# Optimization experiments

Measured on AMD Instinct MI355X. Metric: run time of the kernel, lower is better.

Reference implementation:

```python
import jax, jax.numpy as jnp
import numpy as np

N = 100000          # total nodes
E = 1200000         # total edges
IN_CH = 22          # NUM_NODES_SINGLE_TEAM * 2
HID = 64
NUM_CLASSES = 3
G = 256             # graphs in batch


def setup_inputs() -> dict:
    key = jax.random.key(0)
    ks = jax.random.split(key, 12)
    x = jax.random.normal(ks[0], (N, IN_CH), jnp.float32)
    edge_index = jax.random.randint(ks[1], (2, E), 0, N, dtype=jnp.int32)
    edge_weight = jax.random.uniform(ks[2], (E,), jnp.float32)
    batch = jnp.sort(jax.random.randint(ks[3], (N,), 0, G, dtype=jnp.int32))

    def lin_w(k, fi, fo):
        return jax.random.normal(k, (fi, fo), jnp.float32) / np.float32(np.sqrt(fi))

    return {
        "x": x,
        "edge_index": edge_index,
        "edge_weight": edge_weight,
        "batch": batch,
        "W1": lin_w(ks[4], IN_CH, HID),  "b1": jnp.zeros((HID,), jnp.float32),
        "W2": lin_w(ks[5], HID, HID),    "b2": jnp.zeros((HID,), jnp.float32),
        "fw1": lin_w(ks[6], HID, HID),   "fb1": jnp.zeros((HID,), jnp.float32),
        "fw2": lin_w(ks[7], HID, NUM_CLASSES), "fb2": jnp.zeros((NUM_CLASSES,), jnp.float32),
    }


def gcn_conv(x, edge_index, edge_weight, W, b):
    """PyG GCNConv: self-loops (weight 1) + symmetric normalization + scatter-add."""
    n = x.shape[0]
    loop = jnp.arange(n, dtype=edge_index.dtype)
    row = jnp.concatenate([edge_index[0], loop])
    col = jnp.concatenate([edge_index[1], loop])
    w = jnp.concatenate([edge_weight, jnp.ones((n,), x.dtype)])
    deg = jax.ops.segment_sum(w, col, num_segments=n)        # weighted in-degree
    safe = jnp.where(deg > 0, deg, 1.0)
    dinv = jnp.where(deg > 0, jax.lax.rsqrt(safe), 0.0)
    norm = dinv[row] * w * dinv[col]                         # [E+N]
    h = x @ W                                                # transform first (d small)
    msg = norm[:, None] * h[row]                             # gather + scale
    out = jax.ops.segment_sum(msg, col, num_segments=n)      # scatter-add
    return out + b


def reference(x, edge_index, edge_weight, batch, W1, b1, W2, b2, fw1, fb1, fw2, fb2):
    h = jax.nn.relu(gcn_conv(x, edge_index, edge_weight, W1, b1))
    h = jax.nn.relu(gcn_conv(h, edge_index, edge_weight, W2, b2))
    # global_mean_pool
    sums = jax.ops.segment_sum(h, batch, num_segments=G)
    cnt = jax.ops.segment_sum(jnp.ones((h.shape[0],), h.dtype), batch, num_segments=G)
    pooled = sums / jnp.maximum(cnt, 1.0)[:, None]
    h = jax.nn.relu(pooled @ fw1 + fb1)
    return h @ fw2 + fb2
```

## Files before the change

### kernel.cpp

```cpp
#include <hip/hip_runtime.h>
#include <hip/hip_bf16.h>
#include <hip/hip_fp16.h>


#define HIDC 64
#define MTILE 128
#define XS_STRIDE (MTILE + 4)
#define BSHIFT 9
#define SPAN 512
#define NBKT_MAX 256
#define BCHUNK 2048

typedef unsigned long long u64;

__global__ void k_init(int* bucket_cnt, int nb, float* pooled, int npool) {
    int i = blockIdx.x * blockDim.x + threadIdx.x;
    if (i < nb) bucket_cnt[i] = 0;
    if (i < npool) pooled[i] = 0.f;
}

__global__ __launch_bounds__(256) void k_bin_count(const int* __restrict__ col,
                                                   int* bucket_cnt, int E, int NB) {
    __shared__ int hist[NBKT_MAX];
    int tid = threadIdx.x;
    for (int i = tid; i < NB; i += 256) hist[i] = 0;
    __syncthreads();
    int base = blockIdx.x * 8192;
    for (int j = 0; j < 32; ++j) {
        int e = base + j * 256 + tid;
        if (e < E) atomicAdd(&hist[col[e] >> BSHIFT], 1);
    }
    __syncthreads();
    for (int i = tid; i < NB; i += 256)
        if (hist[i]) atomicAdd(&bucket_cnt[i], hist[i]);
}

__global__ void k_bucket_scan(const int* __restrict__ bucket_cnt, int* __restrict__ bucket_base,
                              int* __restrict__ cursor_g, int NB, int E) {
    __shared__ int s[256];
    int t = threadIdx.x;
    int v = (t < NB) ? bucket_cnt[t] : 0;
    s[t] = v;
    __syncthreads();
    for (int o = 1; o < 256; o <<= 1) {
        int x = (t >= o) ? s[t - o] : 0;
        __syncthreads();
        s[t] += x;
        __syncthreads();
    }
    if (t < NB) { int ex = s[t] - v; bucket_base[t] = ex; cursor_g[t] = ex; }
    if (t == 0) bucket_base[NB] = E;
}

__global__ __launch_bounds__(256) void k_bin_scatter(const int* __restrict__ row,
                                                     const int* __restrict__ col,
                                                     const float* __restrict__ ew,
                                                     int* cursor_g, u64* __restrict__ bedges,
                                                     int E, int NB) {
    __shared__ int hist[NBKT_MAX], binoff[NBKT_MAX], cursor[NBKT_MAX], gbase[NBKT_MAX];
    __shared__ int s[256];
    __shared__ u64 stage[BCHUNK];
    __shared__ unsigned char binid[BCHUNK];
    int tid = threadIdx.x;
    for (int i = tid; i < NB; i += 256) hist[i] = 0;
    __syncthreads();
    int base = blockIdx.x * BCHUNK;
    u64 pk[8]; int bb[8];
#pragma unroll
    for (int j = 0; j < 8; ++j) {
        int e = base + j * 256 + tid;
        if (e < E) {
            int c = col[e];
            bb[j] = c >> BSHIFT;
            pk[j] = ((u64)__float_as_uint(ew[e]) << 32) |
                    ((u64)(unsigned)row[e] << BSHIFT) | (unsigned)(c & (SPAN - 1));
            atomicAdd(&hist[bb[j]], 1);
        } else bb[j] = -1;
    }
    __syncthreads();
    {
        int v = (tid < NB) ? hist[tid] : 0;
        s[tid] = v;
        __syncthreads();
        for (int o = 1; o < 256; o <<= 1) {
            int x = (tid >= o) ? s[tid - o] : 0;
            __syncthreads();
            s[tid] += x;
            __syncthreads();
        }
        if (tid < NB) { binoff[tid] = s[tid] - v; cursor[tid] = s[tid] - v; }
    }
    __syncthreads();
#pragma unroll
    for (int j = 0; j < 8; ++j)
        if (bb[j] >= 0) {
            int pos = atomicAdd(&cursor[bb[j]], 1);
            stage[pos] = pk[j];
            binid[pos] = (unsigned char)bb[j];
        }
    __syncthreads();
    if (tid < NB && hist[tid] > 0) gbase[tid] = atomicAdd(&cursor_g[tid], hist[tid]);
    __syncthreads();
    int total = min(BCHUNK, E - base);
    for (int i = tid; i < total; i += 256) {
        int b = binid[i];
        bedges[(size_t)gbase[b] + (i - binoff[b])] = stage[i];
    }
}

__global__ __launch_bounds__(256) void k_bucket_process(const u64* __restrict__ bedges,
                                                        const int* __restrict__ bucket_base,
                                                        const float* __restrict__ x,
                                                        u64* __restrict__ csr,
                                                        float* __restrict__ dinv,
                                                        int* __restrict__ off,
                                                        __half* __restrict__ x16,
                                                        int N, int E, int NB, int K) {
    __shared__ float deg[SPAN];
    __shared__ int cL[SPAN];
    __shared__ int offL[SPAN];
    __shared__ int s[256];
    int b = blockIdx.x, tid = threadIdx.x;
    int ebase = bucket_base[b], ecnt = bucket_base[b + 1] - ebase;
    int nd0 = b << BSHIFT;
    int ndn = min(SPAN, N - nd0);
    for (int i = tid; i < SPAN; i += 256) { deg[i] = 1.0f; cL[i] = 0; }
    __syncthreads();
    for (int e = tid; e < ecnt; e += 256) {
        u64 p = bedges[ebase + e];
        int colin = (int)(p & (SPAN - 1));
        atomicAdd(&deg[colin], __uint_as_float((unsigned)(p >> 32)));
        atomicAdd(&cL[colin], 1);
    }
    __syncthreads();
    int p0 = cL[2 * tid], p1 = cL[2 * tid + 1];
    s[tid] = p0 + p1;
    __syncthreads();
    for (int o = 1; o < 256; o <<= 1) {
        int x_ = (tid >= o) ? s[tid - o] : 0;
        __syncthreads();
        s[tid] += x_;
        __syncthreads();
    }
    int ex = s[tid] - (p0 + p1);
    offL[2 * tid] = ex;
    offL[2 * tid + 1] = ex + p0;
    __syncthreads();
    for (int i = tid; i < ndn; i += 256) {
        float dv = rsqrtf(deg[i]);
        deg[i] = dv;
        dinv[nd0 + i] = dv;
        off[nd0 + i] = ebase + offL[i];
    }
    for (int i = tid; i < SPAN; i += 256) cL[i] = offL[i];
    if (b == NB - 1 && tid == 0) off[N] = E;
    __syncthreads();
    for (int e = tid; e < ecnt; e += 256) {
        u64 p = bedges[ebase + e];
        int colin = (int)(p & (SPAN - 1));
        int src = (int)((p >> BSHIFT) & 0x7FFFFF);
        int slot = atomicAdd(&cL[colin], 1);
        csr[(size_t)ebase + slot] = ((u64)(unsigned)src << 32) | (unsigned)(p >> 32);
    }
    for (int i = tid; i < ndn * 16; i += 256) {
        int nl = i >> 4, p = i & 15, c0 = p * 2;
        float dv = deg[nl];
        const float* xr = x + (size_t)(nd0 + nl) * K;
        float a = (c0 < K)     ? dv * xr[c0]     : 0.f;
        float bq = (c0 + 1 < K) ? dv * xr[c0 + 1] : 0.f;
        reinterpret_cast<__half2*>(x16)[(size_t)(nd0 + nl) * 16 + p] = __floats2half2_rn(a, bq);
    }
}

__global__ void k_agg_x(const __half* __restrict__ x16, const int* __restrict__ off,
                        const u64* __restrict__ csr, const float* __restrict__ dinv,
                        float* __restrict__ agg, int n, int K) {
    int t = blockIdx.x * blockDim.x + threadIdx.x;
    int lane = threadIdx.x & 63;
    int node = ((t >> 6) << 3) + (lane >> 3);
    int sub = lane & 7;
    if (node >= n) return;
    const uint2* xp = reinterpret_cast<const uint2*>(x16);
    uint2 sv = xp[(size_t)node * 8 + sub];
    float acc0, acc1, acc2, acc3;
    {
        float2 a = __half22float2(*(const __half2*)&sv.x);
        float2 b = __half22float2(*(const __half2*)&sv.y);
        acc0 = a.x; acc1 = a.y; acc2 = b.x; acc3 = b.y;
    }
    int i = off[node], e1 = off[node + 1];
    for (; i + 7 < e1; i += 8) {
        u64 e[8]; uint2 r[8];
#pragma unroll
        for (int j = 0; j < 8; ++j) e[j] = csr[i + j];
#pragma unroll
        for (int j = 0; j < 8; ++j) r[j] = xp[(size_t)(e[j] >> 32) * 8 + sub];
#pragma unroll
        for (int j = 0; j < 8; ++j) {
            float w = __uint_as_float((unsigned)e[j]);
            float2 a = __half22float2(*(const __half2*)&r[j].x);
            float2 b = __half22float2(*(const __half2*)&r[j].y);
            acc0 = fmaf(w, a.x, acc0); acc1 = fmaf(w, a.y, acc1);
            acc2 = fmaf(w, b.x, acc2); acc3 = fmaf(w, b.y, acc3);
        }
    }
    for (; i < e1; ++i) {
        u64 e0 = csr[i];
        uint2 r = xp[(size_t)(e0 >> 32) * 8 + sub];
        float w = __uint_as_float((unsigned)e0);
        float2 a = __half22float2(*(const __half2*)&r.x);
        float2 b = __half22float2(*(const __half2*)&r.y);
        acc0 = fmaf(w, a.x, acc0); acc1 = fmaf(w, a.y, acc1);
        acc2 = fmaf(w, b.x, acc2); acc3 = fmaf(w, b.y, acc3);
    }
    int c0 = sub * 4;
    float d = dinv[node];
    float* ap = agg + (size_t)node * K + c0;
    if (c0 + 3 < K) {
        float2 o0; o0.x = d * acc0; o0.y = d * acc1;
        float2 o1; o1.x = d * acc2; o1.y = d * acc3;
        *reinterpret_cast<float2*>(ap) = o0;
        *reinterpret_cast<float2*>(ap + 2) = o1;
    } else if (c0 < K) {
        float2 o; o.x = d * acc0; o.y = d * acc1;
        *reinterpret_cast<float2*>(ap) = o;
    }
}

template <int K1>
__global__ __launch_bounds__(256) void k_layer1_fused(const float* __restrict__ agg,
                                                      const float* __restrict__ W1,
                                                      const float* __restrict__ b1,
                                                      const float* __restrict__ W2,
                                                      const float* __restrict__ dinv,
                                                      __half* __restrict__ h, int n) {
    __shared__ float smem[HIDC * XS_STRIDE];
    __shared__ float ws[HIDC * HIDC];
    int tid = threadIdx.x;
    int n0 = blockIdx.x * MTILE;

    for (int i = tid; i < K1 * HIDC; i += 256) ws[i] = W1[i];
    for (int i = tid; i < MTILE * K1; i += 256) {
        int r = i / K1, k = i - r * K1;
        smem[k * XS_STRIDE + r] = (n0 + r < n) ? agg[(size_t)(n0 + r) * K1 + k] : 0.f;
    }
    __syncthreads();

    int c0 = (tid & 15) * 4;
    int m0 = (tid >> 4) * 8;
    float acc[8][4];
#pragma unroll
    for (int j = 0; j < 8; ++j)
#pragma unroll
        for (int q = 0; q < 4; ++q) acc[j][q] = 0.f;

#pragma unroll 2
    for (int k = 0; k < K1; ++k) {
        float4 a0 = *reinterpret_cast<const float4*>(&smem[k * XS_STRIDE + m0]);
        float4 a1 = *reinterpret_cast<const float4*>(&smem[k * XS_STRIDE + m0 + 4]);
        float4 b  = *reinterpret_cast<const float4*>(&ws[k * HIDC + c0]);
        float av[8] = {a0.x, a0.y, a0.z, a0.w, a1.x, a1.y, a1.z, a1.w};
        float bv[4] = {b.x, b.y, b.z, b.w};
#pragma unroll
        for (int j = 0; j < 8; ++j)
#pragma unroll
            for (int q = 0; q < 4; ++q)
                acc[j][q] = fmaf(av[j], bv[q], acc[j][q]);
    }

    float4 bb = *reinterpret_cast<const float4*>(b1 + c0);
    float bv4[4] = {bb.x, bb.y, bb.z, bb.w};
#pragma unroll
    for (int j = 0; j < 8; ++j)
#pragma unroll
        for (int q = 0; q < 4; ++q)
            acc[j][q] = fmaxf(acc[j][q] + bv4[q], 0.f);

    __syncthreads();

#pragma unroll
    for (int j = 0; j < 8; ++j)
#pragma unroll
        for (int q = 0; q < 4; ++q)
            smem[(c0 + q) * XS_STRIDE + (m0 + j)] = (n0 + m0 + j < n) ? acc[j][q] : 0.f;
    for (int i = tid; i < HIDC * HIDC; i += 256) ws[i] = W2[i];
    __syncthreads();

#pragma unroll
    for (int j = 0; j < 8; ++j)
#pragma unroll
        for (int q = 0; q < 4; ++q) acc[j][q] = 0.f;

#pragma unroll 2
    for (int k = 0; k < HIDC; ++k) {
        float4 a0 = *reinterpret_cast<const float4*>(&smem[k * XS_STRIDE + m0]);
        float4 a1 = *reinterpret_cast<const float4*>(&smem[k * XS_STRIDE + m0 + 4]);
        float4 b  = *reinterpret_cast<const float4*>(&ws[k * HIDC + c0]);
        float av[8] = {a0.x, a0.y, a0.z, a0.w, a1.x, a1.y, a1.z, a1.w};
        float bv[4] = {b.x, b.y, b.z, b.w};
#pragma unroll
        for (int j = 0; j < 8; ++j)
#pragma unroll
            for (int q = 0; q < 4; ++q)
                acc[j][q] = fmaf(av[j], bv[q], acc[j][q]);
    }

#pragma unroll
    for (int j = 0; j < 8; ++j) {
        int node = n0 + m0 + j;
        if (node < n) {
            float dv = dinv[node];
            union { struct { __half2 a, b; } h2; float2 f2; } u;
            u.h2.a = __floats2half2_rn(acc[j][0] * dv, acc[j][1] * dv);
            u.h2.b = __floats2half2_rn(acc[j][2] * dv, acc[j][3] * dv);
            *reinterpret_cast<float2*>(h + (size_t)node * HIDC + c0) = u.f2;
        }
    }
}

__global__ void k_gcn_gather(const __half* __restrict__ h, const int* __restrict__ off,
                             const u64* __restrict__ csr, const float* __restrict__ dinv,
                             const float* __restrict__ bias, float* __restrict__ out, int n) {
    int t = blockIdx.x * blockDim.x + threadIdx.x;
    int lane = threadIdx.x & 63;
    int node = ((t >> 6) << 2) + (lane >> 4);
    int sub = lane & 15;
    if (node >= n) return;
    const uint2* hp = reinterpret_cast<const uint2*>(h);
    float d = dinv[node];
    uint2 sv = hp[(size_t)node * 16 + sub];
    float acc0, acc1, acc2, acc3;
    {
        float2 a = __half22float2(*(const __half2*)&sv.x);
        float2 b = __half22float2(*(const __half2*)&sv.y);
        acc0 = a.x; acc1 = a.y; acc2 = b.x; acc3 = b.y;
    }
    int i = off[node], e1 = off[node + 1];
    for (; i + 7 < e1; i += 8) {
        u64 e[8]; uint2 r[8];
#pragma unroll
        for (int j = 0; j < 8; ++j) e[j] = csr[i + j];
#pragma unroll
        for (int j = 0; j < 8; ++j) r[j] = hp[(size_t)(e[j] >> 32) * 16 + sub];
#pragma unroll
        for (int j = 0; j < 8; ++j) {
            float w = __uint_as_float((unsigned)e[j]);
            float2 a = __half22float2(*(const __half2*)&r[j].x);
            float2 b = __half22float2(*(const __half2*)&r[j].y);
            acc0 = fmaf(w, a.x, acc0); acc1 = fmaf(w, a.y, acc1);
            acc2 = fmaf(w, b.x, acc2); acc3 = fmaf(w, b.y, acc3);
        }
    }
    for (; i < e1; ++i) {
        u64 e0 = csr[i];
        uint2 r = hp[(size_t)(e0 >> 32) * 16 + sub];
        float w = __uint_as_float((unsigned)e0);
        float2 a = __half22float2(*(const __half2*)&r.x);
        float2 b = __half22float2(*(const __half2*)&r.y);
        acc0 = fmaf(w, a.x, acc0); acc1 = fmaf(w, a.y, acc1);
        acc2 = fmaf(w, b.x, acc2); acc3 = fmaf(w, b.y, acc3);
    }
    int c0 = sub * 4;
    float4 bb = *reinterpret_cast<const float4*>(bias + c0);
    float4 o;
    o.x = fmaxf(fmaf(d, acc0, bb.x), 0.f);
    o.y = fmaxf(fmaf(d, acc1, bb.y), 0.f);
    o.z = fmaxf(fmaf(d, acc2, bb.z), 0.f);
    o.w = fmaxf(fmaf(d, acc3, bb.w), 0.f);
    *reinterpret_cast<float4*>(out + (size_t)node * HIDC + c0) = o;
}

__global__ void k_pool(const float* __restrict__ h, const int* __restrict__ batch,
                       float* __restrict__ pooled, float* __restrict__ cnt, int n) {
    int c = threadIdx.x & 63, sub = threadIdx.x >> 6;
    int n0 = blockIdx.x * 256;
    int nend = min(n0 + 256, n);
    float acc = 0.f, cacc = 0.f;
    int curb = -1;
    for (int i = n0 + sub; i < nend; i += 4) {
        int b = batch[i];
        if (b != curb) {
            if (curb >= 0) {
                atomicAdd(&pooled[curb * HIDC + c], acc);
                if (c == 0) atomicAdd(&cnt[curb], cacc);
            }
            acc = 0.f; cacc = 0.f;
            curb = b;
        }
        acc += h[(size_t)i * HIDC + c];
        cacc += 1.f;
    }
    if (curb >= 0) {
        atomicAdd(&pooled[curb * HIDC + c], acc);
        if (c == 0) atomicAdd(&cnt[curb], cacc);
    }
}

__global__ void k_head(const float* __restrict__ pooled, const float* __restrict__ cnt,
                       const float* __restrict__ fw1, const float* __restrict__ fb1,
                       const float* __restrict__ fw2, const float* __restrict__ fb2,
                       float* __restrict__ out, int nclass) {
    int g = blockIdx.x;
    int j = threadIdx.x;
    __shared__ float p[HIDC], hid[HIDC];
    float c = fmaxf(cnt[g], 1.0f);
    p[j] = pooled[g * HIDC + j] / c;
    __syncthreads();
    float acc = fb1[j];
#pragma unroll 8
    for (int k = 0; k < HIDC; ++k) acc = fmaf(p[k], fw1[k * HIDC + j], acc);
    hid[j] = fmaxf(acc, 0.f);
    __syncthreads();
    if (j < nclass) {
        float o = fb2[j];
#pragma unroll 8
        for (int k = 0; k < HIDC; ++k) o = fmaf(hid[k], fw2[k * nclass + j], o);
        out[g * nclass + j] = o;
    }
}

extern "C" void kernel_launch(void* const* d_in, const int* in_sizes, int n_in,
                              void* d_out, int out_size, void* d_ws, size_t ws_size,
                              hipStream_t stream) {
    const float* x    = (const float*)d_in[0];
    const int* eidx   = (const int*)d_in[1];
    const float* ew   = (const float*)d_in[2];
    const int* batch  = (const int*)d_in[3];
    const float* W1   = (const float*)d_in[4];
    const float* b1   = (const float*)d_in[5];
    const float* W2   = (const float*)d_in[6];
    const float* b2   = (const float*)d_in[7];
    const float* fw1  = (const float*)d_in[8];
    const float* fb1  = (const float*)d_in[9];
    const float* fw2  = (const float*)d_in[10];
    const float* fb2  = (const float*)d_in[11];
    float* out = (float*)d_out;

    const int N = in_sizes[3];
    const int E = in_sizes[1] / 2;
    const int INCH = in_sizes[0] / N;
    const int NCLASS = in_sizes[11];
    const int G = out_size / NCLASS;
    const int NB = (N + SPAN - 1) >> BSHIFT;

    const int* row = eidx;
    const int* col = eidx + E;

    char* wp = (char*)d_ws;
    u64*   bedges = (u64*)wp;    wp += sizeof(u64) * E;
    u64*   csr    = (u64*)wp;    wp += sizeof(u64) * E;
    float* dinv   = (float*)wp;  wp += sizeof(float) * N;
    __half* x16   = (__half*)wp; wp += sizeof(__half) * (size_t)N * 32;
    float* agg    = (float*)wp;  wp += sizeof(float) * (size_t)N * INCH;
    __half* hbuf  = (__half*)wp; wp += sizeof(__half) * (size_t)N * HIDC;
    float* bufB   = (float*)wp;  wp += sizeof(float) * (size_t)N * HIDC;
    float* pooled = (float*)wp;  wp += sizeof(float) * (size_t)G * HIDC;
    float* cnt    = (float*)wp;  wp += sizeof(float) * G;
    int*   off    = (int*)wp;    wp += sizeof(int) * (N + 1);
    int*   bucket_cnt  = (int*)wp; wp += sizeof(int) * NBKT_MAX;
    int*   bucket_base = (int*)wp; wp += sizeof(int) * (NBKT_MAX + 1);
    int*   cursor_g    = (int*)wp; wp += sizeof(int) * NBKT_MAX;

    const int BLK = 256;
    dim3 blk(BLK);
    int gTile   = (N + MTILE - 1) / MTILE;
    int gAggX   = (N + 31) / 32;
    int gGather = (N + 15) / 16;
    int nInit   = max(NB, G * HIDC + G);

    k_init<<<(nInit + BLK - 1) / BLK, blk, 0, stream>>>(bucket_cnt, NB, pooled, G * HIDC + G);

    k_bin_count<<<(E + 8191) / 8192, blk, 0, stream>>>(col, bucket_cnt, E, NB);
    k_bucket_scan<<<1, blk, 0, stream>>>(bucket_cnt, bucket_base, cursor_g, NB, E);
    k_bin_scatter<<<(E + BCHUNK - 1) / BCHUNK, blk, 0, stream>>>(row, col, ew, cursor_g,
                                                                 bedges, E, NB);
    k_bucket_process<<<NB, blk, 0, stream>>>(bedges, bucket_base, x, csr, dinv, off, x16,
                                             N, E, NB, INCH);

    k_agg_x<<<gAggX, blk, 0, stream>>>(x16, off, csr, dinv, agg, N, INCH);
    k_layer1_fused<22><<<gTile, blk, 0, stream>>>(agg, W1, b1, W2, dinv, hbuf, N);

    k_gcn_gather<<<gGather, blk, 0, stream>>>(hbuf, off, csr, dinv, b2, bufB, N);

    k_pool<<<(N + 255) / 256, blk, 0, stream>>>(bufB, batch, pooled, cnt, N);
    k_head<<<G, dim3(64), 0, stream>>>(pooled, cnt, fw1, fb1, fw2, fb2, out, NCLASS);
}
```

Baseline: 201.6 us.

## Halve bucket span and pack degree sum with edge count into one atomic

Shrinks the bucket span from 512 to 256 nodes, which doubles the bucket count to up to 512. The scans now handle two entries per thread and the bin ids are widened to 16 bits to fit. In the bucket-process kernel, the float degree accumulation and the integer count atomics become a single 64-bit shared atomic: a 32.32 fixed-point weight sum in the low 48 bits and the edge count in the high 16 bits. This halves the LDS atomics and doubles the number of process blocks, at the cost of double-precision conversions, 64-bit atomics, and a fixed-point degree that differs slightly from the float sum.

```diff
diff --git a/kernel.cpp b/kernel.cpp
--- a/kernel.cpp
+++ b/kernel.cpp
@@ -6,10 +6,11 @@
 #define HIDC 64
 #define MTILE 128
 #define XS_STRIDE (MTILE + 4)
-#define BSHIFT 9
-#define SPAN 512
-#define NBKT_MAX 256
+#define BSHIFT 8
+#define SPAN 256
+#define NBKT_MAX 512
 #define BCHUNK 2048
+#define SUM_MASK ((1ULL << 48) - 1)
 
 typedef unsigned long long u64;
 
@@ -39,8 +40,10 @@
                               int* __restrict__ cursor_g, int NB, int E) {
     __shared__ int s[256];
     int t = threadIdx.x;
-    int v = (t < NB) ? bucket_cnt[t] : 0;
-    s[t] = v;
+    int i0 = 2 * t, i1 = 2 * t + 1;
+    int v0 = (i0 < NB) ? bucket_cnt[i0] : 0;
+    int v1 = (i1 < NB) ? bucket_cnt[i1] : 0;
+    s[t] = v0 + v1;
     __syncthreads();
     for (int o = 1; o < 256; o <<= 1) {
         int x = (t >= o) ? s[t - o] : 0;
@@ -48,7 +51,9 @@
         s[t] += x;
         __syncthreads();
     }
-    if (t < NB) { int ex = s[t] - v; bucket_base[t] = ex; cursor_g[t] = ex; }
+    int ex = s[t] - (v0 + v1);
+    if (i0 < NB) { bucket_base[i0] = ex;      cursor_g[i0] = ex; }
+    if (i1 < NB) { bucket_base[i1] = ex + v0; cursor_g[i1] = ex + v0; }
     if (t == 0) bucket_base[NB] = E;
 }
 
@@ -60,7 +65,7 @@
     __shared__ int hist[NBKT_MAX], binoff[NBKT_MAX], cursor[NBKT_MAX], gbase[NBKT_MAX];
     __shared__ int s[256];
     __shared__ u64 stage[BCHUNK];
-    __shared__ unsigned char binid[BCHUNK];
+    __shared__ unsigned short binid[BCHUNK];
     int tid = threadIdx.x;
     for (int i = tid; i < NB; i += 256) hist[i] = 0;
     __syncthreads();
@@ -79,8 +84,10 @@
     }
     __syncthreads();
     {
-        int v = (tid < NB) ? hist[tid] : 0;
-        s[tid] = v;
+        int i0 = 2 * tid, i1 = 2 * tid + 1;
+        int v0 = (i0 < NB) ? hist[i0] : 0;
+        int v1 = (i1 < NB) ? hist[i1] : 0;
+        s[tid] = v0 + v1;
         __syncthreads();
         for (int o = 1; o < 256; o <<= 1) {
             int x = (tid >= o) ? s[tid - o] : 0;
@@ -88,7 +95,9 @@
             s[tid] += x;
             __syncthreads();
         }
-        if (tid < NB) { binoff[tid] = s[tid] - v; cursor[tid] = s[tid] - v; }
+        int ex = s[tid] - (v0 + v1);
+        if (i0 < NB) { binoff[i0] = ex;      cursor[i0] = ex; }
+        if (i1 < NB) { binoff[i1] = ex + v0; cursor[i1] = ex + v0; }
     }
     __syncthreads();
 #pragma unroll
@@ -96,10 +105,11 @@
         if (bb[j] >= 0) {
             int pos = atomicAdd(&cursor[bb[j]], 1);
             stage[pos] = pk[j];
-            binid[pos] = (unsigned char)bb[j];
-        }
-    __syncthreads();
-    if (tid < NB && hist[tid] > 0) gbase[tid] = atomicAdd(&cursor_g[tid], hist[tid]);
+            binid[pos] = (unsigned short)bb[j];
+        }
+    __syncthreads();
+    for (int i = tid; i < NB; i += 256)
+        if (hist[i] > 0) gbase[i] = atomicAdd(&cursor_g[i], hist[i]);
     __syncthreads();
     int total = min(BCHUNK, E - base);
     for (int i = tid; i < total; i += 256) {
@@ -116,25 +126,27 @@
                                                         int* __restrict__ off,
                                                         __half* __restrict__ x16,
                                                         int N, int E, int NB, int K) {
-    __shared__ float deg[SPAN];
+    __shared__ u64 degp[SPAN];
     __shared__ int cL[SPAN];
     __shared__ int offL[SPAN];
+    __shared__ float dvL[SPAN];
     __shared__ int s[256];
     int b = blockIdx.x, tid = threadIdx.x;
     int ebase = bucket_base[b], ecnt = bucket_base[b + 1] - ebase;
     int nd0 = b << BSHIFT;
     int ndn = min(SPAN, N - nd0);
-    for (int i = tid; i < SPAN; i += 256) { deg[i] = 1.0f; cL[i] = 0; }
+    degp[tid] = (1ULL << 32);
     __syncthreads();
     for (int e = tid; e < ecnt; e += 256) {
         u64 p = bedges[ebase + e];
         int colin = (int)(p & (SPAN - 1));
-        atomicAdd(&deg[colin], __uint_as_float((unsigned)(p >> 32)));
-        atomicAdd(&cL[colin], 1);
-    }
-    __syncthreads();
-    int p0 = cL[2 * tid], p1 = cL[2 * tid + 1];
-    s[tid] = p0 + p1;
+        float w = __uint_as_float((unsigned)(p >> 32));
+        u64 add = (u64)((double)w * 4294967296.0 + 0.5) | (1ULL << 48);
+        atomicAdd(&degp[colin], add);
+    }
+    __syncthreads();
+    int cnt_t = (int)(degp[tid] >> 48);
+    s[tid] = cnt_t;
     __syncthreads();
     for (int o = 1; o < 256; o <<= 1) {
         int x_ = (tid >= o) ? s[tid - o] : 0;
@@ -142,17 +154,15 @@
         s[tid] += x_;
         __syncthreads();
     }
-    int ex = s[tid] - (p0 + p1);
-    offL[2 * tid] = ex;
-    offL[2 * tid + 1] = ex + p0;
-    __syncthreads();
-    for (int i = tid; i < ndn; i += 256) {
-        float dv = rsqrtf(deg[i]);
-        deg[i] = dv;
-        dinv[nd0 + i] = dv;
-        off[nd0 + i] = ebase + offL[i];
-    }
-    for (int i = tid; i < SPAN; i += 256) cL[i] = offL[i];
+    int ex = s[tid] - cnt_t;
+    offL[tid] = ex;
+    cL[tid] = ex;
+    float dv = rsqrtf((float)((double)(degp[tid] & SUM_MASK) * 2.3283064365386963e-10));
+    dvL[tid] = dv;
+    if (tid < ndn) {
+        dinv[nd0 + tid] = dv;
+        off[nd0 + tid] = ebase + ex;
+    }
     if (b == NB - 1 && tid == 0) off[N] = E;
     __syncthreads();
     for (int e = tid; e < ecnt; e += 256) {
@@ -164,10 +174,10 @@
     }
     for (int i = tid; i < ndn * 16; i += 256) {
         int nl = i >> 4, p = i & 15, c0 = p * 2;
-        float dv = deg[nl];
+        float dq = dvL[nl];
         const float* xr = x + (size_t)(nd0 + nl) * K;
-        float a = (c0 < K)     ? dv * xr[c0]     : 0.f;
-        float bq = (c0 + 1 < K) ? dv * xr[c0 + 1] : 0.f;
+        float a = (c0 < K)     ? dq * xr[c0]     : 0.f;
+        float bq = (c0 + 1 < K) ? dq * xr[c0 + 1] : 0.f;
         reinterpret_cast<__half2*>(x16)[(size_t)(nd0 + nl) * 16 + p] = __floats2half2_rn(a, bq);
     }
 }
```

After: 193.9 us. 1.04x faster.
